# Optimization experiments

Hardware: AMD Instinct MI355X
Metric: run time of the kernel (lower is better)

Reference implementation:

```python
import jax, jax.numpy as jnp
import numpy as np

ALPHA = 0.2
NEG_BIG = -9e15

def setup_inputs() -> dict:
    key = jax.random.key(0)
    k1, k2, k3, k4 = jax.random.split(key, 4)
    B, N, F = 8, 2048, 256
    h = jax.random.normal(k1, (B, N, F), dtype=jnp.float32)
    adj = jax.random.randint(k2, (B, N, N), 0, 2, dtype=jnp.int32)
    W = jax.random.normal(k3, (F, F), dtype=jnp.float32) * (1.414 / jnp.sqrt(F))
    a = jax.random.normal(k4, (2 * F, 1), dtype=jnp.float32) * 0.1
    return {"h": h, "adj": adj, "W": W, "a": a}

def reference(h, adj, W, a):
    F_out = W.shape[1]
    Wh = jnp.einsum('bnf,fo->bno', h, W)            # [B,N,F]
    Wh1 = Wh @ a[:F_out]                             # [B,N,1]
    Wh2 = Wh @ a[F_out:]                             # [B,N,1]
    e = jax.nn.leaky_relu(Wh1 + jnp.swapaxes(Wh2, 1, 2), negative_slope=ALPHA)  # [B,N,N]
    scores = jnp.where(adj > 0, e, NEG_BIG)
    attention = jax.nn.softmax(scores, axis=-1)      # [B,N,N]
    h_prime = jnp.einsum('bnm,bmf->bnf', attention, Wh)
    out = h + jax.nn.elu(h_prime)                    # concat=True -> elu; residual add
    return (out, attention)
```

## Files before the change

### kernel.cpp

```cpp
#include <hip/hip_runtime.h>

#define NB 8
#define NN 2048
#define NF 256

typedef __attribute__((ext_vector_type(8))) short bf16x8;
typedef __attribute__((ext_vector_type(4))) float f32x4;

__device__ __forceinline__ unsigned short f2bf(float x) {
  union { float f; unsigned int i; } c; c.f = x;
  unsigned int r = c.i + 0x7FFFu + ((c.i >> 16) & 1u);
  return (unsigned short)(r >> 16);
}
__device__ __forceinline__ unsigned short f2bf_fast(float x) {
  union { float f; unsigned int i; } c; c.f = x;
  return (unsigned short)((c.i + 0x8000u) >> 16);
}
__device__ __forceinline__ bf16x8 cvt8(float4 c0, float4 c1) {
  union { bf16x8 v8; unsigned short us[8]; } cu;
  cu.us[0] = f2bf_fast(c0.x); cu.us[1] = f2bf_fast(c0.y);
  cu.us[2] = f2bf_fast(c0.z); cu.us[3] = f2bf_fast(c0.w);
  cu.us[4] = f2bf_fast(c1.x); cu.us[5] = f2bf_fast(c1.y);
  cu.us[6] = f2bf_fast(c1.z); cu.us[7] = f2bf_fast(c1.w);
  return cu.v8;
}

__global__ __launch_bounds__(256) void k_prep(
    const float* __restrict__ W, const float* __restrict__ a,
    unsigned short* __restrict__ WT, float* __restrict__ u, float* __restrict__ v) {
  int t = threadIdx.x;
  if (blockIdx.x < 256) {
    int k = blockIdx.x;
    WT[t * 256 + k] = f2bf(W[k * 256 + t]);
  } else {
    float su = 0.f, sv = 0.f;
    for (int o = 0; o < 256; ++o) {
      float w = W[t * 256 + o];
      su += w * a[o];
      sv += w * a[256 + o];
    }
    u[t] = su; v[t] = sv;
  }
}

__global__ __launch_bounds__(256) void k_mid(
    const float* __restrict__ h, const unsigned short* __restrict__ WTr,
    const float* __restrict__ u, const float* __restrict__ v,
    unsigned short* __restrict__ WhT, float* __restrict__ Wh1, float* __restrict__ Wh2) {
  int bx = blockIdx.x;
  if (bx < 256) {
    int b = bx >> 5;
    int i64 = (bx & 31) * 64;
    int wave = threadIdx.x >> 6, lane = threadIdx.x & 63;
    int iW = i64 + wave * 16;
    int l15 = lane & 15, q8 = (lane >> 4) * 8;
    const float* hB = h + (size_t)b * NN * NF;

    f32x4 acc[16];
#pragma unroll
    for (int ft = 0; ft < 16; ++ft) acc[ft] = (f32x4){0.f, 0.f, 0.f, 0.f};

    for (int k0 = 0; k0 < NF; k0 += 32) {
      int kk = k0 + q8;
      const float* p = hB + (size_t)(iW + l15) * NF + kk;
      bf16x8 bfr = cvt8(*(const float4*)p, *(const float4*)(p + 4));
#pragma unroll
      for (int ft = 0; ft < 16; ++ft) {
        bf16x8 af = *(const bf16x8*)(WTr + (ft * 16 + l15) * 256 + kk);
        acc[ft] = __builtin_amdgcn_mfma_f32_16x16x32_bf16(af, bfr, acc[ft], 0, 0, 0);
      }
    }

    unsigned short* WhTb = WhT + (size_t)b * NF * NN;
    int q4 = (lane >> 4) * 4;
#pragma unroll
    for (int ft = 0; ft < 16; ++ft)
#pragma unroll
      for (int r = 0; r < 4; ++r) {
        int f = ft * 16 + q4 + r;
        int i = iW + l15;
        WhTb[(size_t)f * NN + i] = f2bf(acc[ft][r]);
      }
  } else {
    int row = (bx - 256) * 4 + (threadIdx.x >> 6);
    int lane = threadIdx.x & 63;
    float4 hv = *(const float4*)(h + (size_t)row * NF + lane * 4);
    const float* up = u + lane * 4;
    const float* vp = v + lane * 4;
    float su = hv.x * up[0] + hv.y * up[1] + hv.z * up[2] + hv.w * up[3];
    float sv = hv.x * vp[0] + hv.y * vp[1] + hv.z * vp[2] + hv.w * vp[3];
#pragma unroll
    for (int off = 32; off >= 1; off >>= 1) {
      su += __shfl_xor(su, off);
      sv += __shfl_xor(sv, off);
    }
    if (lane == 0) { Wh1[row] = su; Wh2[row] = sv; }
  }
}

__global__ __launch_bounds__(512, 4) void k_fuse(
    const int* __restrict__ adj, const float* __restrict__ Wh1,
    const float* __restrict__ Wh2, const unsigned short* __restrict__ WhT,
    const float* __restrict__ h, float* __restrict__ att, float* __restrict__ out) {
  __shared__ unsigned short satt[16 * 2048];
  const float NEGBIG = -9.0e15f;
  int bx = blockIdx.x;
  bx = (bx & 7) * 128 + (bx >> 3);
  int b = bx >> 7;
  int i0 = (bx & 127) * 16;
  int wave = threadIdx.x >> 6, lane = threadIdx.x & 63;
  const float* w2 = Wh2 + ((size_t)b << 11);

  int rowbase = b * NN + i0 + wave * 2;
#pragma unroll
  for (int rr = 0; rr < 2; ++rr) {
    const int* arow = adj + (size_t)(rowbase + rr) * NN;
    float w1 = Wh1[rowbase + rr];
    float x[32];
#pragma unroll
    for (int c = 0; c < 8; ++c) {
      int j = c * 256 + lane * 4;
      int4 av = *(const int4*)(arow + j);
      float4 pv = *(const float4*)(w2 + j);
      float t;
      t = w1 + pv.x; t = t >= 0.f ? t : 0.2f * t; x[c*4+0] = (av.x > 0) ? t : NEGBIG;
      t = w1 + pv.y; t = t >= 0.f ? t : 0.2f * t; x[c*4+1] = (av.y > 0) ? t : NEGBIG;
      t = w1 + pv.z; t = t >= 0.f ? t : 0.2f * t; x[c*4+2] = (av.z > 0) ? t : NEGBIG;
      t = w1 + pv.w; t = t >= 0.f ? t : 0.2f * t; x[c*4+3] = (av.w > 0) ? t : NEGBIG;
    }

    float m = x[0];
#pragma unroll
    for (int k = 1; k < 32; ++k) m = fmaxf(m, x[k]);
#pragma unroll
    for (int off = 32; off >= 1; off >>= 1) m = fmaxf(m, __shfl_xor(m, off));
    float sum = 0.f;
#pragma unroll
    for (int k = 0; k < 32; ++k) { x[k] = __expf(x[k] - m); sum += x[k]; }
#pragma unroll
    for (int off = 32; off >= 1; off >>= 1) sum += __shfl_xor(sum, off);
    float iv = 1.0f / sum;

    int row_local = wave * 2 + rr;
    int swz = row_local * 8;
    float* orow = att + (size_t)(rowbase + rr) * NN;
    unsigned short* srow = satt + row_local * 2048;
#pragma unroll
    for (int c = 0; c < 8; ++c) {
      int j = c * 256 + lane * 4;
      float a0 = x[c*4+0] * iv, a1 = x[c*4+1] * iv;
      float a2 = x[c*4+2] * iv, a3 = x[c*4+3] * iv;
      *(float4*)(orow + j) = make_float4(a0, a1, a2, a3);
      int e = ((j & ~7) ^ swz) + (j & 7);
      union { short4 v4; unsigned short us[4]; } pk;
      pk.us[0] = f2bf_fast(a0); pk.us[1] = f2bf_fast(a1);
      pk.us[2] = f2bf_fast(a2); pk.us[3] = f2bf_fast(a3);
      *(short4*)(srow + e) = pk.v4;
    }
  }

  __syncthreads();

  int fW = wave * 32;
  int l15 = lane & 15, q8 = (lane >> 4) * 8;
  const unsigned short* WTb = WhT + (size_t)b * NF * NN;
  const unsigned short* aRow = satt + l15 * 2048;
  int swzA = l15 * 8;

  f32x4 acc[2];
#pragma unroll
  for (int nt = 0; nt < 2; ++nt) acc[nt] = (f32x4){0.f, 0.f, 0.f, 0.f};

  for (int kk = 0; kk < NN; kk += 32) {
    bf16x8 afr = *(const bf16x8*)(aRow + (((kk + q8) ^ swzA)));
    bf16x8 bfr[2];
#pragma unroll
    for (int nt = 0; nt < 2; ++nt) {
      int f = fW + nt * 16 + l15;
      bfr[nt] = *(const bf16x8*)(WTb + (size_t)f * NN + kk + q8);
    }
#pragma unroll
    for (int nt = 0; nt < 2; ++nt)
      acc[nt] = __builtin_amdgcn_mfma_f32_16x16x32_bf16(afr, bfr[nt], acc[nt], 0, 0, 0);
  }

  int q4 = (lane >> 4) * 4;
#pragma unroll
  for (int nt = 0; nt < 2; ++nt)
#pragma unroll
    for (int r = 0; r < 4; ++r) {
      int i = i0 + q4 + r;
      int f = fW + nt * 16 + l15;
      size_t idx = ((size_t)(b * NN + i)) * NF + f;
      float hp = acc[nt][r];
      float el = hp > 0.f ? hp : expm1f(hp);
      out[idx] = h[idx] + el;
    }
}

extern "C" void kernel_launch(void* const* d_in, const int* in_sizes, int n_in,
                              void* d_out, int out_size, void* d_ws, size_t ws_size,
                              hipStream_t stream) {
  const float* h = nullptr; const int* adj = nullptr;
  const float* W = nullptr; const float* a = nullptr;
  for (int i = 0; i < n_in; ++i) {
    int s = in_sizes[i];
    if (s == NB * NN * NF) h = (const float*)d_in[i];
    else if (s == NB * NN * NN) adj = (const int*)d_in[i];
    else if (s == NF * NF) W = (const float*)d_in[i];
    else if (s == 2 * NF) a = (const float*)d_in[i];
  }

  float* out = (float*)d_out;
  float* att = out + (size_t)NB * NN * NF;

  char* ws = (char*)d_ws;
  unsigned short* WhT = (unsigned short*)ws;
  unsigned short* WTr = (unsigned short*)(ws + 8388608);
  float* u   = (float*)(ws + 8388608 + 131072);
  float* v   = u + 256;
  float* Wh1 = v + 256;
  float* Wh2 = Wh1 + NB * NN;

  k_prep<<<257, 256, 0, stream>>>(W, a, WTr, u, v);
  k_mid<<<256 + NB * NN / 4, 256, 0, stream>>>(h, WTr, u, v, WhT, Wh1, Wh2);
  k_fuse<<<NB * 128, 512, 0, stream>>>(adj, Wh1, Wh2, WhT, h, att, out);
}
```

Baseline: 412.9 us.

## Retile Wh projection, fold Wh1/Wh2 dots into it, and use nontemporal streaming

The Wh projection kernel is retiled so each block handles 16 rows across all 256 features, with four waves each covering 64 features, giving 1024 blocks instead of 256. The separate Wh1/Wh2 row-dot blocks are removed; wave 0 computes those dots from the h values it already loads for the MFMA. In the fused attention kernel, the adj reads, attention writes and the h/out residual accesses now use nontemporal loads and stores to avoid polluting cache with streamed data. The dot-product reduction now runs serially inside wave 0, and h is read redundantly by all four waves.

```diff
diff --git a/kernel.cpp b/kernel.cpp
--- a/kernel.cpp
+++ b/kernel.cpp
@@ -6,6 +6,7 @@
 
 typedef __attribute__((ext_vector_type(8))) short bf16x8;
 typedef __attribute__((ext_vector_type(4))) float f32x4;
+typedef __attribute__((ext_vector_type(4))) int i32x4;
 
 __device__ __forceinline__ unsigned short f2bf(float x) {
   union { float f; unsigned int i; } c; c.f = x;
@@ -17,6 +18,14 @@
   return (unsigned short)((c.i + 0x8000u) >> 16);
 }
 __device__ __forceinline__ bf16x8 cvt8(float4 c0, float4 c1) {
+  union { bf16x8 v8; unsigned short us[8]; } cu;
+  cu.us[0] = f2bf_fast(c0.x); cu.us[1] = f2bf_fast(c0.y);
+  cu.us[2] = f2bf_fast(c0.z); cu.us[3] = f2bf_fast(c0.w);
+  cu.us[4] = f2bf_fast(c1.x); cu.us[5] = f2bf_fast(c1.y);
+  cu.us[6] = f2bf_fast(c1.z); cu.us[7] = f2bf_fast(c1.w);
+  return cu.v8;
+}
+__device__ __forceinline__ bf16x8 cvt8v(f32x4 c0, f32x4 c1) {
   union { bf16x8 v8; unsigned short us[8]; } cu;
   cu.us[0] = f2bf_fast(c0.x); cu.us[1] = f2bf_fast(c0.y);
   cu.us[2] = f2bf_fast(c0.z); cu.us[3] = f2bf_fast(c0.w);
@@ -48,53 +57,56 @@
     const float* __restrict__ u, const float* __restrict__ v,
     unsigned short* __restrict__ WhT, float* __restrict__ Wh1, float* __restrict__ Wh2) {
   int bx = blockIdx.x;
-  if (bx < 256) {
-    int b = bx >> 5;
-    int i64 = (bx & 31) * 64;
-    int wave = threadIdx.x >> 6, lane = threadIdx.x & 63;
-    int iW = i64 + wave * 16;
-    int l15 = lane & 15, q8 = (lane >> 4) * 8;
-    const float* hB = h + (size_t)b * NN * NF;
-
-    f32x4 acc[16];
-#pragma unroll
-    for (int ft = 0; ft < 16; ++ft) acc[ft] = (f32x4){0.f, 0.f, 0.f, 0.f};
-
-    for (int k0 = 0; k0 < NF; k0 += 32) {
-      int kk = k0 + q8;
-      const float* p = hB + (size_t)(iW + l15) * NF + kk;
-      bf16x8 bfr = cvt8(*(const float4*)p, *(const float4*)(p + 4));
-#pragma unroll
-      for (int ft = 0; ft < 16; ++ft) {
-        bf16x8 af = *(const bf16x8*)(WTr + (ft * 16 + l15) * 256 + kk);
-        acc[ft] = __builtin_amdgcn_mfma_f32_16x16x32_bf16(af, bfr, acc[ft], 0, 0, 0);
-      }
-    }
-
-    unsigned short* WhTb = WhT + (size_t)b * NF * NN;
-    int q4 = (lane >> 4) * 4;
-#pragma unroll
-    for (int ft = 0; ft < 16; ++ft)
-#pragma unroll
-      for (int r = 0; r < 4; ++r) {
-        int f = ft * 16 + q4 + r;
-        int i = iW + l15;
-        WhTb[(size_t)f * NN + i] = f2bf(acc[ft][r]);
-      }
-  } else {
-    int row = (bx - 256) * 4 + (threadIdx.x >> 6);
-    int lane = threadIdx.x & 63;
-    float4 hv = *(const float4*)(h + (size_t)row * NF + lane * 4);
-    const float* up = u + lane * 4;
-    const float* vp = v + lane * 4;
-    float su = hv.x * up[0] + hv.y * up[1] + hv.z * up[2] + hv.w * up[3];
-    float sv = hv.x * vp[0] + hv.y * vp[1] + hv.z * vp[2] + hv.w * vp[3];
-#pragma unroll
-    for (int off = 32; off >= 1; off >>= 1) {
-      su += __shfl_xor(su, off);
-      sv += __shfl_xor(sv, off);
-    }
-    if (lane == 0) { Wh1[row] = su; Wh2[row] = sv; }
+  int b = bx >> 7;
+  int iW = (bx & 127) * 16;
+  int wave = threadIdx.x >> 6, lane = threadIdx.x & 63;
+  int fW = wave * 64;
+  int l15 = lane & 15, q8 = (lane >> 4) * 8;
+  const float* hB = h + (size_t)b * NN * NF;
+
+  f32x4 acc[4];
+#pragma unroll
+  for (int ft = 0; ft < 4; ++ft) acc[ft] = (f32x4){0.f, 0.f, 0.f, 0.f};
+  float su = 0.f, sv = 0.f;
+
+  for (int k0 = 0; k0 < NF; k0 += 32) {
+    int kk = k0 + q8;
+    const float* p = hB + (size_t)(iW + l15) * NF + kk;
+    float4 h0 = *(const float4*)p;
+    float4 h1 = *(const float4*)(p + 4);
+    bf16x8 bfr = cvt8(h0, h1);
+    if (wave == 0) {
+      const float* up = u + kk;
+      const float* vp = v + kk;
+      su += h0.x*up[0] + h0.y*up[1] + h0.z*up[2] + h0.w*up[3]
+          + h1.x*up[4] + h1.y*up[5] + h1.z*up[6] + h1.w*up[7];
+      sv += h0.x*vp[0] + h0.y*vp[1] + h0.z*vp[2] + h0.w*vp[3]
+          + h1.x*vp[4] + h1.y*vp[5] + h1.z*vp[6] + h1.w*vp[7];
+    }
+#pragma unroll
+    for (int ft = 0; ft < 4; ++ft) {
+      bf16x8 af = *(const bf16x8*)(WTr + (fW + ft * 16 + l15) * 256 + kk);
+      acc[ft] = __builtin_amdgcn_mfma_f32_16x16x32_bf16(af, bfr, acc[ft], 0, 0, 0);
+    }
+  }
+
+  unsigned short* WhTb = WhT + (size_t)b * NF * NN;
+  int q4 = (lane >> 4) * 4;
+#pragma unroll
+  for (int ft = 0; ft < 4; ++ft)
+#pragma unroll
+    for (int r = 0; r < 4; ++r) {
+      int f = fW + ft * 16 + q4 + r;
+      WhTb[(size_t)f * NN + iW + l15] = f2bf(acc[ft][r]);
+    }
+
+  if (wave == 0) {
+    su += __shfl_xor(su, 16); su += __shfl_xor(su, 32);
+    sv += __shfl_xor(sv, 16); sv += __shfl_xor(sv, 32);
+    if (lane < 16) {
+      Wh1[b * NN + iW + lane] = su;
+      Wh2[b * NN + iW + lane] = sv;
+    }
   }
 }
 
@@ -120,7 +132,7 @@
 #pragma unroll
     for (int c = 0; c < 8; ++c) {
       int j = c * 256 + lane * 4;
-      int4 av = *(const int4*)(arow + j);
+      i32x4 av = __builtin_nontemporal_load((const i32x4*)(arow + j));
       float4 pv = *(const float4*)(w2 + j);
       float t;
       t = w1 + pv.x; t = t >= 0.f ? t : 0.2f * t; x[c*4+0] = (av.x > 0) ? t : NEGBIG;
@@ -150,7 +162,8 @@
       int j = c * 256 + lane * 4;
       float a0 = x[c*4+0] * iv, a1 = x[c*4+1] * iv;
       float a2 = x[c*4+2] * iv, a3 = x[c*4+3] * iv;
-      *(float4*)(orow + j) = make_float4(a0, a1, a2, a3);
+      f32x4 ov = (f32x4){a0, a1, a2, a3};
+      __builtin_nontemporal_store(ov, (f32x4*)(orow + j));
       int e = ((j & ~7) ^ swz) + (j & 7);
       union { short4 v4; unsigned short us[4]; } pk;
       pk.us[0] = f2bf_fast(a0); pk.us[1] = f2bf_fast(a1);
@@ -194,7 +207,8 @@
       size_t idx = ((size_t)(b * NN + i)) * NF + f;
       float hp = acc[nt][r];
       float el = hp > 0.f ? hp : expm1f(hp);
-      out[idx] = h[idx] + el;
+      float hv = __builtin_nontemporal_load(h + idx);
+      __builtin_nontemporal_store(hv + el, out + idx);
     }
 }
 
@@ -223,6 +237,6 @@
   float* Wh2 = Wh1 + NB * NN;
 
   k_prep<<<257, 256, 0, stream>>>(W, a, WTr, u, v);
-  k_mid<<<256 + NB * NN / 4, 256, 0, stream>>>(h, WTr, u, v, WhT, Wh1, Wh2);
+  k_mid<<<1024, 256, 0, stream>>>(h, WTr, u, v, WhT, Wh1, Wh2);
   k_fuse<<<NB * 128, 512, 0, stream>>>(adj, Wh1, Wh2, WhT, h, att, out);
 }
```

New measurement: 406.7 us. About the same (-1.5%).
